# Kernel optimization log

Measured on AMD Instinct MI355X. Metric: run time of the kernel, lower is better.

Reference implementation:

```python
import jax, jax.numpy as jnp
import numpy as np

N_NODES = 122880  # 4096 graphs * 30 nodes
N_EDGES = 983040


def gcn_conv(x, W, b, src, dst, n):
    """PyG GCNConv: symmetric-normalized aggregation with self-loops."""
    h = x @ W  # [n, out]
    loop = jnp.arange(n, dtype=src.dtype)
    s = jnp.concatenate([src, loop])
    d = jnp.concatenate([dst, loop])
    deg = jnp.zeros((n,), dtype=h.dtype).at[d].add(1.0)  # >=1 due to self loops
    dinv = jax.lax.rsqrt(deg)
    norm = dinv[s] * dinv[d]  # [E+n]
    out = jax.ops.segment_sum(h[s] * norm[:, None], d, num_segments=n)
    return out + b


def setup_inputs() -> dict:
    key = jax.random.key(0)
    ks = jax.random.split(key, 8)
    x = jax.random.normal(ks[0], (N_NODES, 64), dtype=jnp.float32)
    edge_index = jax.random.randint(ks[1], (2, N_EDGES), 0, N_NODES, dtype=jnp.int64)
    W1 = jax.random.normal(ks[2], (64, 128), dtype=jnp.float32) * (1.0 / np.sqrt(64))
    b1 = jnp.zeros((128,), dtype=jnp.float32)
    W2 = jax.random.normal(ks[3], (128, 64), dtype=jnp.float32) * (1.0 / np.sqrt(128))
    b2 = jnp.zeros((64,), dtype=jnp.float32)
    Wfc = jax.random.normal(ks[4], (1920, 1728), dtype=jnp.float32) * (1.0 / np.sqrt(1920))
    bfc = jnp.zeros((1728,), dtype=jnp.float32)
    return {"x": x, "edge_index": edge_index, "W1": W1, "b1": b1,
            "W2": W2, "b2": b2, "Wfc": Wfc, "bfc": bfc}


def reference(x, edge_index, W1, b1, W2, b2, Wfc, bfc):
    n = x.shape[0]
    src, dst = edge_index[0], edge_index[1]
    h = gcn_conv(x, W1, b1, src, dst, n)
    h = jax.nn.relu(h)  # dropout is identity in eval mode
    h = gcn_conv(h, W2, b2, src, dst, n)
    h = jax.nn.relu(h)
    h = h.reshape(-1, 64 * 30)  # [B, 1920], 30 nodes per graph
    return h @ Wfc + bfc  # [B, 1728]
```

## Files before the change

kernel.cpp:

```cpp
#include <hip/hip_runtime.h>
#include <hip/hip_bf16.h>

#define N_NODES 122880
#define N_EDGES 983040
#define NBKT 480
#define BCAP 2560
#define EPB 4096
#define NPAD 1792

typedef __hip_bfloat16 bf16;
typedef __attribute__((ext_vector_type(8))) short short8;
typedef __attribute__((ext_vector_type(4))) float floatx4;

__device__ __forceinline__ void gl_lds16(const void* g, void* l) {
    __builtin_amdgcn_global_load_lds(
        (const __attribute__((address_space(1))) void*)g,
        (__attribute__((address_space(3))) void*)l, 16, 0, 0);
}

__device__ __forceinline__ float bflo(unsigned u) {
    return __uint_as_float(u << 16);
}
__device__ __forceinline__ float bfhi(unsigned u) {
    return __uint_as_float(u & 0xffff0000u);
}

__global__ __launch_bounds__(256) void k_psort(const int* __restrict__ ei,
                                               int* __restrict__ gcur,
                                               unsigned* __restrict__ gbuf) {
    __shared__ int cur[NBKT];
    __shared__ int gb[NBKT];
    const int t = threadIdx.x;
    for (int i = t; i < NBKT; i += 256) cur[i] = 0;
    __syncthreads();
    const int base = blockIdx.x * EPB;
    unsigned pay[16];
    short bk[16], pib[16];
#pragma unroll
    for (int j = 0; j < 16; ++j) {
        int e = base + j * 256 + t;
        int d = ei[N_EDGES + e];
        int s = ei[e];
        bk[j] = (short)(d >> 8);
        pay[j] = (unsigned)(d & 255) | ((unsigned)s << 8);
        pib[j] = (short)atomicAdd(&cur[d >> 8], 1);
    }
    __syncthreads();
    for (int i = t; i < NBKT; i += 256) {
        int c = cur[i];
        gb[i] = c ? atomicAdd(&gcur[i * 16], c) : 0;
    }
    __syncthreads();
#pragma unroll
    for (int j = 0; j < 16; ++j) {
        int pos = gb[bk[j]] + pib[j];
        if (pos < BCAP) gbuf[bk[j] * BCAP + pos] = pay[j];
    }
}

__global__ __launch_bounds__(256) void k_bcsr(const int* __restrict__ gcur,
                                              const unsigned* __restrict__ gbuf,
                                              int* __restrict__ adj,
                                              unsigned* __restrict__ co,
                                              float* __restrict__ dinv) {
    __shared__ int hist[256];
    __shared__ int arr[256];
    __shared__ int exc[256];
    const int b = blockIdx.x, t = threadIdx.x;
    hist[t] = 0;
    __syncthreads();
    int E = gcur[b * 16];
    if (E > BCAP) E = BCAP;
    int dl[10], sv[10];
    short pb[10];
    int n = 0;
    for (int idx = t; idx < E; idx += 256) {
        unsigned p = gbuf[b * BCAP + idx];
        dl[n] = p & 255;
        sv[n] = (int)(p >> 8);
        pb[n] = (short)atomicAdd(&hist[dl[n]], 1);
        ++n;
    }
    __syncthreads();
    const int cnt_t = hist[t];
    arr[t] = cnt_t;
    __syncthreads();
    for (int d = 1; d < 256; d <<= 1) {
        int v = (t >= d) ? arr[t - d] : 0;
        __syncthreads();
        arr[t] += v;
        __syncthreads();
    }
    const int ex = arr[t] - cnt_t;
    exc[t] = ex;
    const int node = b * 256 + t;
    co[node] = ((unsigned)ex << 16) | (unsigned)cnt_t;
    dinv[node] = rsqrtf((float)cnt_t + 1.0f);
    __syncthreads();
    for (int j = 0; j < n; ++j)
        adj[b * BCAP + exc[dl[j]] + pb[j]] = sv[j];
}

__global__ __launch_bounds__(256) void k_xtobf(const float* __restrict__ x,
                                               bf16* __restrict__ xb) {
    int t = blockIdx.x * 256 + threadIdx.x;
    const float4 v = ((const float4*)x)[t];
    bf16* o = xb + t * 4;
    o[0] = __float2bfloat16(v.x);
    o[1] = __float2bfloat16(v.y);
    o[2] = __float2bfloat16(v.z);
    o[3] = __float2bfloat16(v.w);
}

__global__ __launch_bounds__(256) void k_convw(const float* __restrict__ W1,
                                               const float* __restrict__ W2,
                                               bf16* __restrict__ W1T,
                                               bf16* __restrict__ W2T) {
    int t = blockIdx.x * 256 + threadIdx.x;
    if (t < 64 * 128) {
        int k = t >> 7, n = t & 127;
        W1T[n * 64 + k] = __float2bfloat16(W1[t]);
    } else {
        int u = t - 64 * 128;
        int k = u >> 6, n = u & 63;
        W2T[n * 128 + k] = __float2bfloat16(W2[u]);
    }
}

__global__ __launch_bounds__(256) void k_transWfc(const float* __restrict__ W,
                                                  bf16* __restrict__ WT) {
    __shared__ float t[32][33];
    int tx = threadIdx.x, ty = threadIdx.y;
    int n0 = blockIdx.x * 32, k0 = blockIdx.y * 32;
    const bool nok = (n0 + tx) < 1728;
#pragma unroll
    for (int j = 0; j < 4; ++j)
        t[ty + j * 8][tx] =
            nok ? W[(long)(k0 + ty + j * 8) * 1728 + n0 + tx] : 0.0f;
    __syncthreads();
#pragma unroll
    for (int j = 0; j < 4; ++j)
        WT[(long)(n0 + ty + j * 8) * 1920 + k0 + tx] =
            __float2bfloat16(t[tx][ty + j * 8]);
}

template <bool BIAS_RELU>
__global__ __launch_bounds__(256) void k_agg(const bf16* __restrict__ xb,
                                             const float* __restrict__ dinv,
                                             const unsigned* __restrict__ co,
                                             const int* __restrict__ adj,
                                             const float* __restrict__ bias,
                                             bf16* __restrict__ out) {
    const int wave = threadIdx.x >> 6, lane = threadIdx.x & 63;
    const int sub = lane >> 4, l16 = lane & 15;
    const int node = blockIdx.x * 16 + wave * 4 + sub;

    const float di = dinv[node];
    const unsigned c_ = co[node];
    int c = (int)(c_ & 0xffffu);
    if (c > 32) c = 32;
    const int* al = adj + (node >> 8) * BCAP + (c_ >> 16);
    int   sl  = (l16 < c)      ? al[l16]      : 0;
    int   sl2 = (16 + l16 < c) ? al[16 + l16] : 0;
    float wl  = (l16 < c)      ? dinv[sl]     : 0.0f;
    float wl2 = (16 + l16 < c) ? dinv[sl2]    : 0.0f;

    const uint2 us = *(const uint2*)(xb + ((long)node << 6) + (l16 << 2));
    float a0 = di * bflo(us.x), a1 = di * bfhi(us.x);
    float a2 = di * bflo(us.y), a3 = di * bfhi(us.y);

    for (int p0 = 0; p0 < c; p0 += 8) {
        uint2 uu[8];
        float w8[8];
#pragma unroll
        for (int j = 0; j < 8; ++j) {
            int p = p0 + j;
            bool ok = p < c;
            int   sv = (p < 16) ? sl : sl2;
            float wv = (p < 16) ? wl : wl2;
            int s = ok ? __shfl(sv, p & 15, 16) : 0;
            w8[j] = ok ? __shfl(wv, p & 15, 16) : 0.0f;
            uu[j] = *(const uint2*)(xb + ((long)s << 6) + (l16 << 2));
        }
#pragma unroll
        for (int j = 0; j < 8; ++j) {
            a0 += w8[j] * bflo(uu[j].x);
            a1 += w8[j] * bfhi(uu[j].x);
            a2 += w8[j] * bflo(uu[j].y);
            a3 += w8[j] * bfhi(uu[j].y);
        }
    }

    float r0 = di * a0, r1 = di * a1, r2 = di * a2, r3 = di * a3;
    if (BIAS_RELU) {
        r0 = fmaxf(r0 + bias[l16 * 4 + 0], 0.0f);
        r1 = fmaxf(r1 + bias[l16 * 4 + 1], 0.0f);
        r2 = fmaxf(r2 + bias[l16 * 4 + 2], 0.0f);
        r3 = fmaxf(r3 + bias[l16 * 4 + 3], 0.0f);
    }
    bf16* o = out + ((long)node << 6) + (l16 << 2);
    o[0] = __float2bfloat16(r0);
    o[1] = __float2bfloat16(r1);
    o[2] = __float2bfloat16(r2);
    o[3] = __float2bfloat16(r3);
}

__global__ __launch_bounds__(256) void k_mlp(const bf16* __restrict__ xa,
                                             const bf16* __restrict__ W1T,
                                             const bf16* __restrict__ W2T,
                                             const float* __restrict__ b1,
                                             bf16* __restrict__ g) {
    __shared__ __align__(16) bf16 As[128 * 64];
    __shared__ __align__(16) bf16 C1s[128 * 136];
    const int tid = threadIdx.x;
    const int wave = tid >> 6, lane = tid & 63;
    const int quad = lane >> 4, l16 = lane & 15;
    const int bm = blockIdx.x * 128;
    const int wm = (wave & 1) * 64;
    const int wn1 = (wave >> 1) * 64;
    const int wn2 = (wave >> 1) * 32;

#pragma unroll
    for (int q = 0; q < 4; ++q) {
        int G = q * 256 + tid;
        int gc = (G & ~7) | ((G & 7) ^ ((G >> 3) & 7));
        gl_lds16(xa + (long)bm * 64 + gc * 8, As + ((q * 4 + wave) * 64) * 8);
    }
    short8 w1f[2][4];
#pragma unroll
    for (int kc = 0; kc < 2; ++kc)
#pragma unroll
        for (int in = 0; in < 4; ++in)
            w1f[kc][in] = *(const short8*)(W1T + (wn1 + in * 16 + l16) * 64 +
                                           kc * 32 + quad * 8);
    floatx4 acc1[4][4];
#pragma unroll
    for (int i = 0; i < 4; ++i)
#pragma unroll
        for (int j = 0; j < 4; ++j) acc1[i][j] = (floatx4){0.f, 0.f, 0.f, 0.f};
    __syncthreads();

#pragma unroll
    for (int kc = 0; kc < 2; ++kc)
#pragma unroll
        for (int im = 0; im < 4; ++im) {
            const int R = wm + im * 16 + l16;
            short8 af = *(const short8*)(As + R * 64 +
                                         (((kc * 4 + quad) ^ (R & 7)) * 8));
#pragma unroll
            for (int in = 0; in < 4; ++in)
                acc1[im][in] = __builtin_amdgcn_mfma_f32_16x16x32_bf16(
                    af, w1f[kc][in], acc1[im][in], 0, 0, 0);
        }

#pragma unroll
    for (int in = 0; in < 4; ++in) {
        const int col = wn1 + in * 16 + l16;
        const float bv = b1[col];
#pragma unroll
        for (int im = 0; im < 4; ++im) {
            const int row = wm + im * 16 + quad * 4;
#pragma unroll
            for (int r = 0; r < 4; ++r)
                C1s[(row + r) * 136 + col] =
                    __float2bfloat16(fmaxf(acc1[im][in][r] + bv, 0.0f));
        }
    }
    short8 w2f[4][2];
#pragma unroll
    for (int kc = 0; kc < 4; ++kc)
#pragma unroll
        for (int in = 0; in < 2; ++in)
            w2f[kc][in] = *(const short8*)(W2T + (wn2 + in * 16 + l16) * 128 +
                                           kc * 32 + quad * 8);
    floatx4 acc2[4][2];
#pragma unroll
    for (int i = 0; i < 4; ++i)
#pragma unroll
        for (int j = 0; j < 2; ++j) acc2[i][j] = (floatx4){0.f, 0.f, 0.f, 0.f};
    __syncthreads();

#pragma unroll
    for (int kc = 0; kc < 4; ++kc)
#pragma unroll
        for (int im = 0; im < 4; ++im) {
            short8 af = *(const short8*)(C1s + (wm + im * 16 + l16) * 136 +
                                         kc * 32 + quad * 8);
#pragma unroll
            for (int in = 0; in < 2; ++in)
                acc2[im][in] = __builtin_amdgcn_mfma_f32_16x16x32_bf16(
                    af, w2f[kc][in], acc2[im][in], 0, 0, 0);
        }

#pragma unroll
    for (int in = 0; in < 2; ++in) {
        const int col = wn2 + in * 16 + l16;
#pragma unroll
        for (int im = 0; im < 4; ++im) {
            const int row = bm + wm + im * 16 + quad * 4;
#pragma unroll
            for (int r = 0; r < 4; ++r)
                g[(long)(row + r) * 64 + col] = __float2bfloat16(acc2[im][in][r]);
        }
    }
}

template <bool RELU, bool BIAS, typename OutT>
__global__ __launch_bounds__(256) void gemm_bt(const bf16* __restrict__ A,
                                               const bf16* __restrict__ BT,
                                               const float* __restrict__ bias,
                                               OutT* __restrict__ C,
                                               int M, int N, int K) {
    __shared__ __align__(16) bf16 As[2][128 * 32];
    __shared__ __align__(16) bf16 Bs[2][128 * 32];
    const int tid = threadIdx.x;
    const int wave = tid >> 6, lane = tid & 63;
    const int quad = lane >> 4, l16 = lane & 15;
    const int bid = blockIdx.x;
    const int bx = (bid & 7) * 4 + ((bid >> 3) & 3);
    const int by = bid >> 5;
    const int bm = bx * 128, bn = by * 128;
    const int wm = (wave & 1) * 64, wn = (wave >> 1) * 64;

    floatx4 acc[4][4];
#pragma unroll
    for (int i = 0; i < 4; ++i)
#pragma unroll
        for (int j = 0; j < 4; ++j) acc[i][j] = (floatx4){0.f, 0.f, 0.f, 0.f};

    const int r4 = tid >> 2;
    const int cc = tid & 3;
    const int slot = r4 * 32 + ((cc ^ ((r4 >> 1) & 3)) * 8);

    const bf16* gA0 = A + (long)(bm + r4) * K + cc * 8;
    const bf16* gA1 = A + (long)(bm + r4 + 64) * K + cc * 8;
    const bf16* gB0 = BT + (long)(bn + r4) * K + cc * 8;
    const bf16* gB1 = BT + (long)(bn + r4 + 64) * K + cc * 8;

    const int rsw = (l16 >> 1) & 3;
    const int NT = K >> 5;

    uint4 ra0 = *(const uint4*)gA0;
    uint4 ra1 = *(const uint4*)gA1;
    uint4 rb0 = *(const uint4*)gB0;
    uint4 rb1 = *(const uint4*)gB1;
    *(uint4*)(As[0] + slot) = ra0;
    *(uint4*)(As[0] + 2048 + slot) = ra1;
    *(uint4*)(Bs[0] + slot) = rb0;
    *(uint4*)(Bs[0] + 2048 + slot) = rb1;
    ra0 = *(const uint4*)(gA0 + 32);
    ra1 = *(const uint4*)(gA1 + 32);
    rb0 = *(const uint4*)(gB0 + 32);
    rb1 = *(const uint4*)(gB1 + 32);
    __syncthreads();

    for (int t = 0; t < NT; t += 2) {
        {
            short8 af[4], bfr[4];
#pragma unroll
            for (int im = 0; im < 4; ++im)
                af[im] = *(const short8*)(As[0] + (wm + im * 16 + l16) * 32 +
                                          (quad ^ rsw) * 8);
#pragma unroll
            for (int in = 0; in < 4; ++in)
                bfr[in] = *(const short8*)(Bs[0] + (wn + in * 16 + l16) * 32 +
                                           (quad ^ rsw) * 8);
            *(uint4*)(As[1] + slot) = ra0;
            *(uint4*)(As[1] + 2048 + slot) = ra1;
            *(uint4*)(Bs[1] + slot) = rb0;
            *(uint4*)(Bs[1] + 2048 + slot) = rb1;
            if (t + 2 < NT) {
                ra0 = *(const uint4*)(gA0 + (t + 2) * 32);
                ra1 = *(const uint4*)(gA1 + (t + 2) * 32);
                rb0 = *(const uint4*)(gB0 + (t + 2) * 32);
                rb1 = *(const uint4*)(gB1 + (t + 2) * 32);
            }
#pragma unroll
            for (int im = 0; im < 4; ++im)
#pragma unroll
                for (int in = 0; in < 4; ++in)
                    acc[im][in] = __builtin_amdgcn_mfma_f32_16x16x32_bf16(
                        af[im], bfr[in], acc[im][in], 0, 0, 0);
            __syncthreads();
        }
        {
            short8 af[4], bfr[4];
#pragma unroll
            for (int im = 0; im < 4; ++im)
                af[im] = *(const short8*)(As[1] + (wm + im * 16 + l16) * 32 +
                                          (quad ^ rsw) * 8);
#pragma unroll
            for (int in = 0; in < 4; ++in)
                bfr[in] = *(const short8*)(Bs[1] + (wn + in * 16 + l16) * 32 +
                                           (quad ^ rsw) * 8);
            if (t + 2 < NT) {
                *(uint4*)(As[0] + slot) = ra0;
                *(uint4*)(As[0] + 2048 + slot) = ra1;
                *(uint4*)(Bs[0] + slot) = rb0;
                *(uint4*)(Bs[0] + 2048 + slot) = rb1;
            }
            if (t + 3 < NT) {
                ra0 = *(const uint4*)(gA0 + (t + 3) * 32);
                ra1 = *(const uint4*)(gA1 + (t + 3) * 32);
                rb0 = *(const uint4*)(gB0 + (t + 3) * 32);
                rb1 = *(const uint4*)(gB1 + (t + 3) * 32);
            }
#pragma unroll
            for (int im = 0; im < 4; ++im)
#pragma unroll
                for (int in = 0; in < 4; ++in)
                    acc[im][in] = __builtin_amdgcn_mfma_f32_16x16x32_bf16(
                        af[im], bfr[in], acc[im][in], 0, 0, 0);
            __syncthreads();
        }
    }

#pragma unroll
    for (int in = 0; in < 4; ++in) {
        int gcol = bn + wn + in * 16 + l16;
        bool wok = gcol < N;
        float bv = (BIAS && wok) ? bias[gcol] : 0.0f;
#pragma unroll
        for (int im = 0; im < 4; ++im) {
            int mrow = bm + wm + im * 16 + quad * 4;
#pragma unroll
            for (int r = 0; r < 4; ++r) {
                float v = acc[im][in][r] + bv;
                if (RELU) v = fmaxf(v, 0.0f);
                if (wok) {
                    if constexpr (sizeof(OutT) == 2)
                        C[(long)(mrow + r) * N + gcol] = __float2bfloat16(v);
                    else
                        C[(long)(mrow + r) * N + gcol] = v;
                }
            }
        }
    }
}

extern "C" void kernel_launch(void* const* d_in, const int* in_sizes, int n_in,
                              void* d_out, int out_size, void* d_ws, size_t ws_size,
                              hipStream_t stream) {
    const float* x   = (const float*)d_in[0];
    const int*   ei  = (const int*)d_in[1];
    const float* W1  = (const float*)d_in[2];
    const float* b1  = (const float*)d_in[3];
    const float* W2  = (const float*)d_in[4];
    const float* b2  = (const float*)d_in[5];
    const float* Wfc = (const float*)d_in[6];
    const float* bfc = (const float*)d_in[7];

    char* p = (char*)d_ws;
    int*      gcur = (int*)p;      p += (size_t)NBKT * 16 * 4;
    unsigned* gbuf = (unsigned*)p; p += (size_t)NBKT * BCAP * 4;
    int*      adj  = (int*)p;      p += (size_t)NBKT * BCAP * 4;
    unsigned* co   = (unsigned*)p; p += (size_t)N_NODES * 4;
    float*    dinv = (float*)p;    p += (size_t)N_NODES * 4;
    bf16*     xb   = (bf16*)p;     p += (size_t)N_NODES * 64 * 2;
    bf16*     xa   = (bf16*)p;     p += (size_t)N_NODES * 64 * 2;
    bf16*     g    = (bf16*)p;     p += (size_t)N_NODES * 64 * 2;
    bf16*     h2   = (bf16*)p;     p += (size_t)N_NODES * 64 * 2;
    bf16*     W1T  = (bf16*)p;     p += 128 * 64 * 2;
    bf16*     W2T  = (bf16*)p;     p += 64 * 128 * 2;
    bf16*     WfcT = (bf16*)p;     p += (size_t)NPAD * 1920 * 2;

    hipMemsetAsync(gcur, 0, (size_t)NBKT * 16 * 4, stream);
    k_psort<<<N_EDGES / EPB, 256, 0, stream>>>(ei, gcur, gbuf);
    k_bcsr<<<NBKT, 256, 0, stream>>>(gcur, gbuf, adj, co, dinv);
    k_xtobf<<<N_NODES * 64 / 4 / 256, 256, 0, stream>>>(x, xb);
    k_convw<<<64, 256, 0, stream>>>(W1, W2, W1T, W2T);
    k_transWfc<<<dim3(56, 60), dim3(32, 8), 0, stream>>>(Wfc, WfcT);

    k_agg<false><<<N_NODES / 16, 256, 0, stream>>>(xb, dinv, co, adj, nullptr, xa);
    k_mlp<<<N_NODES / 128, 256, 0, stream>>>(xa, W1T, W2T, b1, g);
    k_agg<true><<<N_NODES / 16, 256, 0, stream>>>(g, dinv, co, adj, b2, h2);
    gemm_bt<false, true, float><<<448, 256, 0, stream>>>(
        h2, WfcT, bfc, (float*)d_out, 4096, 1728, 1920);
}
```

Measured before the change: 238.2 us.

## Fold source-side dinv into features and widen FC GEMM to 512 threads

The source-side normalization dinv[src] is moved out of the aggregation. x is pre-scaled by dinv during the bf16 conversion, and the MLP output g is scaled by dinv in k_mlp's epilogue. k_agg then sums neighbor rows without per-edge weight gathers or weight shuffles, which removes the random dinv loads. Separately, the final GEMM now runs 512 threads per block, each wave covering a 64x32 tile with half the accumulators and one A/B load per thread per stage. This raises occupancy but adds more waves contending at each barrier, and pre-scaling before bf16 rounding slightly changes numerics.

```diff
diff --git a/kernel.cpp b/kernel.cpp
--- a/kernel.cpp
+++ b/kernel.cpp
@@ -102,14 +102,16 @@
 }
 
 __global__ __launch_bounds__(256) void k_xtobf(const float* __restrict__ x,
+                                               const float* __restrict__ dinv,
                                                bf16* __restrict__ xb) {
     int t = blockIdx.x * 256 + threadIdx.x;
+    const float di = dinv[t >> 4];
     const float4 v = ((const float4*)x)[t];
     bf16* o = xb + t * 4;
-    o[0] = __float2bfloat16(v.x);
-    o[1] = __float2bfloat16(v.y);
-    o[2] = __float2bfloat16(v.z);
-    o[3] = __float2bfloat16(v.w);
+    o[0] = __float2bfloat16(di * v.x);
+    o[1] = __float2bfloat16(di * v.y);
+    o[2] = __float2bfloat16(di * v.z);
+    o[3] = __float2bfloat16(di * v.w);
 }
 
 __global__ __launch_bounds__(256) void k_convw(const float* __restrict__ W1,
@@ -160,34 +162,31 @@
     int c = (int)(c_ & 0xffffu);
     if (c > 32) c = 32;
     const int* al = adj + (node >> 8) * BCAP + (c_ >> 16);
-    int   sl  = (l16 < c)      ? al[l16]      : 0;
-    int   sl2 = (16 + l16 < c) ? al[16 + l16] : 0;
-    float wl  = (l16 < c)      ? dinv[sl]     : 0.0f;
-    float wl2 = (16 + l16 < c) ? dinv[sl2]    : 0.0f;
+    int sl  = (l16 < c)      ? al[l16]      : 0;
+    int sl2 = (16 + l16 < c) ? al[16 + l16] : 0;
 
     const uint2 us = *(const uint2*)(xb + ((long)node << 6) + (l16 << 2));
-    float a0 = di * bflo(us.x), a1 = di * bfhi(us.x);
-    float a2 = di * bflo(us.y), a3 = di * bfhi(us.y);
+    float a0 = bflo(us.x), a1 = bfhi(us.x);
+    float a2 = bflo(us.y), a3 = bfhi(us.y);
 
     for (int p0 = 0; p0 < c; p0 += 8) {
         uint2 uu[8];
-        float w8[8];
 #pragma unroll
         for (int j = 0; j < 8; ++j) {
             int p = p0 + j;
             bool ok = p < c;
-            int   sv = (p < 16) ? sl : sl2;
-            float wv = (p < 16) ? wl : wl2;
-            int s = ok ? __shfl(sv, p & 15, 16) : 0;
-            w8[j] = ok ? __shfl(wv, p & 15, 16) : 0.0f;
-            uu[j] = *(const uint2*)(xb + ((long)s << 6) + (l16 << 2));
+            int sv = (p < 16) ? sl : sl2;
+            int s = __shfl(sv, p & 15, 16);
+            uint2 u = *(const uint2*)(xb + ((long)s << 6) + (l16 << 2));
+            uu[j].x = ok ? u.x : 0u;
+            uu[j].y = ok ? u.y : 0u;
         }
 #pragma unroll
         for (int j = 0; j < 8; ++j) {
-            a0 += w8[j] * bflo(uu[j].x);
-            a1 += w8[j] * bfhi(uu[j].x);
-            a2 += w8[j] * bflo(uu[j].y);
-            a3 += w8[j] * bfhi(uu[j].y);
+            a0 += bflo(uu[j].x);
+            a1 += bfhi(uu[j].x);
+            a2 += bflo(uu[j].y);
+            a3 += bfhi(uu[j].y);
         }
     }
 
@@ -209,6 +208,7 @@
                                              const bf16* __restrict__ W1T,
                                              const bf16* __restrict__ W2T,
                                              const float* __restrict__ b1,
+                                             const float* __restrict__ dinv,
                                              bf16* __restrict__ g) {
     __shared__ __align__(16) bf16 As[128 * 64];
     __shared__ __align__(16) bf16 C1s[128 * 136];
@@ -292,6 +292,13 @@
                     af, w2f[kc][in], acc2[im][in], 0, 0, 0);
         }
 
+    float dv[4][4];
+#pragma unroll
+    for (int im = 0; im < 4; ++im)
+#pragma unroll
+        for (int r = 0; r < 4; ++r)
+            dv[im][r] = dinv[bm + wm + im * 16 + quad * 4 + r];
+
 #pragma unroll
     for (int in = 0; in < 2; ++in) {
         const int col = wn2 + in * 16 + l16;
@@ -300,13 +307,14 @@
             const int row = bm + wm + im * 16 + quad * 4;
 #pragma unroll
             for (int r = 0; r < 4; ++r)
-                g[(long)(row + r) * 64 + col] = __float2bfloat16(acc2[im][in][r]);
+                g[(long)(row + r) * 64 + col] =
+                    __float2bfloat16(dv[im][r] * acc2[im][in][r]);
         }
     }
 }
 
 template <bool RELU, bool BIAS, typename OutT>
-__global__ __launch_bounds__(256) void gemm_bt(const bf16* __restrict__ A,
+__global__ __launch_bounds__(512) void gemm_bt(const bf16* __restrict__ A,
                                                const bf16* __restrict__ BT,
                                                const float* __restrict__ bias,
                                                OutT* __restrict__ C,
@@ -320,95 +328,79 @@
     const int bx = (bid & 7) * 4 + ((bid >> 3) & 3);
     const int by = bid >> 5;
     const int bm = bx * 128, bn = by * 128;
-    const int wm = (wave & 1) * 64, wn = (wave >> 1) * 64;
-
-    floatx4 acc[4][4];
+    const int wm = (wave & 1) * 64, wn = (wave >> 1) * 32;
+
+    floatx4 acc[4][2];
 #pragma unroll
     for (int i = 0; i < 4; ++i)
 #pragma unroll
-        for (int j = 0; j < 4; ++j) acc[i][j] = (floatx4){0.f, 0.f, 0.f, 0.f};
+        for (int j = 0; j < 2; ++j) acc[i][j] = (floatx4){0.f, 0.f, 0.f, 0.f};
 
     const int r4 = tid >> 2;
     const int cc = tid & 3;
     const int slot = r4 * 32 + ((cc ^ ((r4 >> 1) & 3)) * 8);
 
-    const bf16* gA0 = A + (long)(bm + r4) * K + cc * 8;
-    const bf16* gA1 = A + (long)(bm + r4 + 64) * K + cc * 8;
-    const bf16* gB0 = BT + (long)(bn + r4) * K + cc * 8;
-    const bf16* gB1 = BT + (long)(bn + r4 + 64) * K + cc * 8;
+    const bf16* gA = A + (long)(bm + r4) * K + cc * 8;
+    const bf16* gB = BT + (long)(bn + r4) * K + cc * 8;
 
     const int rsw = (l16 >> 1) & 3;
     const int NT = K >> 5;
 
-    uint4 ra0 = *(const uint4*)gA0;
-    uint4 ra1 = *(const uint4*)gA1;
-    uint4 rb0 = *(const uint4*)gB0;
-    uint4 rb1 = *(const uint4*)gB1;
-    *(uint4*)(As[0] + slot) = ra0;
-    *(uint4*)(As[0] + 2048 + slot) = ra1;
-    *(uint4*)(Bs[0] + slot) = rb0;
-    *(uint4*)(Bs[0] + 2048 + slot) = rb1;
-    ra0 = *(const uint4*)(gA0 + 32);
-    ra1 = *(const uint4*)(gA1 + 32);
-    rb0 = *(const uint4*)(gB0 + 32);
-    rb1 = *(const uint4*)(gB1 + 32);
+    uint4 ra = *(const uint4*)gA;
+    uint4 rb = *(const uint4*)gB;
+    *(uint4*)(As[0] + slot) = ra;
+    *(uint4*)(Bs[0] + slot) = rb;
+    ra = *(const uint4*)(gA + 32);
+    rb = *(const uint4*)(gB + 32);
     __syncthreads();
 
     for (int t = 0; t < NT; t += 2) {
         {
-            short8 af[4], bfr[4];
+            short8 af[4], bfr[2];
 #pragma unroll
             for (int im = 0; im < 4; ++im)
                 af[im] = *(const short8*)(As[0] + (wm + im * 16 + l16) * 32 +
                                           (quad ^ rsw) * 8);
 #pragma unroll
-            for (int in = 0; in < 4; ++in)
+            for (int in = 0; in < 2; ++in)
                 bfr[in] = *(const short8*)(Bs[0] + (wn + in * 16 + l16) * 32 +
                                            (quad ^ rsw) * 8);
-            *(uint4*)(As[1] + slot) = ra0;
-            *(uint4*)(As[1] + 2048 + slot) = ra1;
-            *(uint4*)(Bs[1] + slot) = rb0;
-            *(uint4*)(Bs[1] + 2048 + slot) = rb1;
+            *(uint4*)(As[1] + slot) = ra;
+            *(uint4*)(Bs[1] + slot) = rb;
             if (t + 2 < NT) {
-                ra0 = *(const uint4*)(gA0 + (t + 2) * 32);
-                ra1 = *(const uint4*)(gA1 + (t + 2) * 32);
-                rb0 = *(const uint4*)(gB0 + (t + 2) * 32);
-                rb1 = *(const uint4*)(gB1 + (t + 2) * 32);
+                ra = *(const uint4*)(gA + (t + 2) * 32);
+                rb = *(const uint4*)(gB + (t + 2) * 32);
             }
 #pragma unroll
             for (int im = 0; im < 4; ++im)
 #pragma unroll
-                for (int in = 0; in < 4; ++in)
+                for (int in = 0; in < 2; ++in)
                     acc[im][in] = __builtin_amdgcn_mfma_f32_16x16x32_bf16(
                         af[im], bfr[in], acc[im][in], 0, 0, 0);
             __syncthreads();
         }
         {
-            short8 af[4], bfr[4];
+            short8 af[4], bfr[2];
 #pragma unroll
             for (int im = 0; im < 4; ++im)
                 af[im] = *(const short8*)(As[1] + (wm + im * 16 + l16) * 32 +
                                           (quad ^ rsw) * 8);
 #pragma unroll
-            for (int in = 0; in < 4; ++in)
+            for (int in = 0; in < 2; ++in)
                 bfr[in] = *(const short8*)(Bs[1] + (wn + in * 16 + l16) * 32 +
                                            (quad ^ rsw) * 8);
             if (t + 2 < NT) {
-                *(uint4*)(As[0] + slot) = ra0;
-                *(uint4*)(As[0] + 2048 + slot) = ra1;
-                *(uint4*)(Bs[0] + slot) = rb0;
-                *(uint4*)(Bs[0] + 2048 + slot) = rb1;
+                *(uint4*)(As[0] + slot) = ra;
+                *(uint4*)(Bs[0] + slot) = rb;
             }
             if (t + 3 < NT) {
-                ra0 = *(const uint4*)(gA0 + (t + 3) * 32);
-                ra1 = *(const uint4*)(gA1 + (t + 3) * 32);
-                rb0 = *(const uint4*)(gB0 + (t + 3) * 32);
-                rb1 = *(const uint4*)(gB1 + (t + 3) * 32);
+                ra = *(const uint4*)(gA + (t + 3) * 32);
+                rb = *(const uint4*)(gB + (t + 3) * 32);
             }
 #pragma unroll
             for (int im = 0; im < 4; ++im)
 #pragma unroll
-                for (int in = 0; in < 4; ++in)
+                for (int in = 0; in < 2; ++in)
                     acc[im][in] = __builtin_amdgcn_mfma_f32_16x16x32_bf16(
                         af[im], bfr[in], acc[im][in], 0, 0, 0);
             __syncthreads();
@@ -416,7 +408,7 @@
     }
 
 #pragma unroll
-    for (int in = 0; in < 4; ++in) {
+    for (int in = 0; in < 2; ++in) {
         int gcol = bn + wn + in * 16 + l16;
         bool wok = gcol < N;
         float bv = (BIAS && wok) ? bias[gcol] : 0.0f;
@@ -467,13 +459,13 @@
     hipMemsetAsync(gcur, 0, (size_t)NBKT * 16 * 4, stream);
     k_psort<<<N_EDGES / EPB, 256, 0, stream>>>(ei, gcur, gbuf);
     k_bcsr<<<NBKT, 256, 0, stream>>>(gcur, gbuf, adj, co, dinv);
-    k_xtobf<<<N_NODES * 64 / 4 / 256, 256, 0, stream>>>(x, xb);
+    k_xtobf<<<N_NODES * 64 / 4 / 256, 256, 0, stream>>>(x, dinv, xb);
     k_convw<<<64, 256, 0, stream>>>(W1, W2, W1T, W2T);
     k_transWfc<<<dim3(56, 60), dim3(32, 8), 0, stream>>>(Wfc, WfcT);
 
     k_agg<false><<<N_NODES / 16, 256, 0, stream>>>(xb, dinv, co, adj, nullptr, xa);
-    k_mlp<<<N_NODES / 128, 256, 0, stream>>>(xa, W1T, W2T, b1, g);
+    k_mlp<<<N_NODES / 128, 256, 0, stream>>>(xa, W1T, W2T, b1, dinv, g);
     k_agg<true><<<N_NODES / 16, 256, 0, stream>>>(g, dinv, co, adj, b2, h2);
-    gemm_bt<false, true, float><<<448, 256, 0, stream>>>(
+    gemm_bt<false, true, float><<<448, 512, 0, stream>>>(
         h2, WfcT, bfc, (float*)d_out, 4096, 1728, 1920);
 }
```

Result: faster. 232.2 us (-2.5%).
